# Kernel optimization log

Hardware: AMD Instinct MI355X
Metric: run time of the kernel (lower is better)

## Reference

```python
import jax, jax.numpy as jnp
import numpy as np

ALPHA = 0.25
GAMMA = 2.0
VAR = jnp.array([0.1, 0.1, 0.2, 0.2, 0.1, 0.1, 0.2, 0.2], dtype=jnp.float32)


def calc_iou(a, b):
    # a: [A,4] anchors, b: [M,4] gt boxes -> IoU [A,M]
    area = (b[:, 2] - b[:, 0]) * (b[:, 3] - b[:, 1])
    iw = jnp.maximum(jnp.minimum(a[:, 2:3], b[:, 2]) - jnp.maximum(a[:, 0:1], b[:, 0]), 0.0)
    ih = jnp.maximum(jnp.minimum(a[:, 3:4], b[:, 3]) - jnp.maximum(a[:, 1:2], b[:, 1]), 0.0)
    ua = jnp.maximum(((a[:, 2] - a[:, 0]) * (a[:, 3] - a[:, 1]))[:, None] + area - iw * ih, 1e-8)
    return iw * ih / ua


def _per_sample(cls_p, reg, anchor, ann1, ann2):
    A = anchor.shape[0]
    M = ann1.shape[0]
    C = cls_p.shape[1]
    clsp = jnp.clip(cls_p, 1e-4, 1.0 - 1e-4)
    iou = calc_iou(anchor, ann1[:, :4])               # [A,M]
    bto = jnp.max(iou, axis=1)                        # best_truth_overlap [A]
    bti = jnp.argmax(iou, axis=1)                     # best_truth_idx [A]
    bpi = jnp.argmax(iou, axis=0)                     # best_prior_idx [M]
    bto = bto.at[bpi].set(2.0)
    owner = jnp.full((A,), -1, jnp.int32).at[bpi].max(jnp.arange(M, dtype=jnp.int32))
    bti = jnp.where(owner >= 0, owner, bti.astype(jnp.int32))
    pos = bto >= 0.5
    neg = bto < 0.4
    assigned = ann1[bti]                              # [A,6]
    labels = assigned[:, 4].astype(jnp.int32)
    onehot = jax.nn.one_hot(labels, C, dtype=clsp.dtype)
    targets = jnp.where(neg[:, None], 0.0, -1.0)
    targets = jnp.where(pos[:, None], onehot, targets)
    af = jnp.where(targets == 1.0, ALPHA, 1.0 - ALPHA)
    fw = af * jnp.where(targets == 1.0, 1.0 - clsp, clsp) ** GAMMA
    bce = -(targets * jnp.log(clsp) + (1.0 - targets) * jnp.log(1.0 - clsp))
    cls_loss = jnp.where(targets != -1.0, fw * bce, 0.0)
    npos = jnp.sum(pos).astype(clsp.dtype)
    cls_out = cls_loss.sum() / jnp.maximum(npos, 1.0)

    aw = anchor[:, 2] - anchor[:, 0]
    ah = anchor[:, 3] - anchor[:, 1]
    acx = anchor[:, 0] + 0.5 * aw
    acy = anchor[:, 1] + 0.5 * ah
    # track-id first-match between frames (replaces nested python loops)
    match = assigned[:, 5][:, None] == ann2[:, 5][None, :]   # [A,M2]
    has = jnp.any(match, axis=1)
    first = jnp.argmax(match, axis=1)
    ann_next = jnp.where(has[:, None], ann2[first], 0.0)     # [A,6]
    gw0 = assigned[:, 2] - assigned[:, 0]
    gh0 = assigned[:, 3] - assigned[:, 1]
    gcx = assigned[:, 0] + 0.5 * gw0
    gcy = assigned[:, 1] + 0.5 * gh0
    gw = jnp.maximum(gw0, 1.0)
    gh = jnp.maximum(gh0, 1.0)
    nw0 = ann_next[:, 2] - ann_next[:, 0]
    nh0 = ann_next[:, 3] - ann_next[:, 1]
    ncx = ann_next[:, 0] + 0.5 * nw0
    ncy = ann_next[:, 1] + 0.5 * nh0
    nw = jnp.maximum(nw0, 1.0)
    nh = jnp.maximum(nh0, 1.0)
    t = jnp.stack([
        (gcx - acx) / aw, (gcy - acy) / ah, jnp.log(gw / aw), jnp.log(gh / ah),
        (ncx - acx) / aw, (ncy - acy) / ah, jnp.log(nw / aw), jnp.log(nh / ah)
    ], axis=1) / VAR                                          # [A,8]
    reg_mask = jnp.concatenate([
        jnp.ones((A, 4), clsp.dtype),
        jnp.broadcast_to(has[:, None], (A, 4)).astype(clsp.dtype)
    ], axis=1)
    diff = jnp.abs(t - reg) * reg_mask
    hub = jnp.where(diff <= 1.0 / 9.0, 0.5 * 9.0 * diff ** 2, diff - 0.5 / 9.0)
    reg_out = jnp.sum(hub * pos[:, None].astype(clsp.dtype)) / jnp.maximum(npos * 8.0, 1.0)
    return cls_out, reg_out


def reference(classifications, regressions, anchors, annotations1, annotations2):
    cl, rl = jax.vmap(_per_sample, in_axes=(0, 0, None, 0, 0))(
        classifications, regressions, anchors[0], annotations1, annotations2)
    return jnp.mean(cl, keepdims=True), jnp.mean(rl, keepdims=True)


def setup_inputs() -> dict:
    key = jax.random.key(0)
    ks = jax.random.split(key, 10)
    B, A, C, M = 8, 100000, 80, 32
    IMG = 512.0

    def rand_boxes(k, prefix):
        k1, k2 = jax.random.split(k)
        ctr = jax.random.uniform(k1, prefix + (2,), jnp.float32, 0.0, IMG)
        wh = jax.random.uniform(k2, prefix + (2,), jnp.float32, 16.0, 128.0)
        return jnp.concatenate([ctr - 0.5 * wh, ctr + 0.5 * wh], axis=-1)

    anchors = rand_boxes(ks[0], (1, A))
    classifications = jax.random.uniform(ks[1], (B, A, C), jnp.float32)
    regressions = jax.random.normal(ks[2], (B, A, 8), jnp.float32) * 0.1

    def make_ann(kb, ki):
        boxes = rand_boxes(kb, (B, M))
        lbl = jax.random.randint(ki, (B, M, 1), 0, C).astype(jnp.float32)
        tid = jax.random.randint(jax.random.fold_in(ki, 1), (B, M, 1), 0, 40).astype(jnp.float32)
        return jnp.concatenate([boxes, lbl, tid], axis=-1)

    annotations1 = make_ann(ks[3], ks[4])
    annotations2 = make_ann(ks[5], ks[6])
    return {"classifications": classifications, "regressions": regressions,
            "anchors": anchors, "annotations1": annotations1, "annotations2": annotations2}
```

## Files before the change

kernel.cpp:

```cpp
#include <hip/hip_runtime.h>

typedef unsigned long long ull;

#define MMAX 128

__global__ void k_init(ull* __restrict__ bpi, int* __restrict__ npos,
                       float* __restrict__ cls_sum, float* __restrict__ reg_sum,
                       int BM, int B) {
    int i = blockIdx.x * blockDim.x + threadIdx.x;
    if (i < BM) bpi[i] = 0ull;
    if (i < B) { npos[i] = 0; cls_sum[i] = 0.f; reg_sum[i] = 0.f; }
}

__global__ void k_iou(const float* __restrict__ anchors, const float* __restrict__ ann1,
                      float* __restrict__ bto, int* __restrict__ bti, ull* __restrict__ bpi,
                      int A, int M) {
    __shared__ float s_box[MMAX][4];
    __shared__ float s_area[MMAX];
    __shared__ ull s_part[4][MMAX];
    const int b = blockIdx.y;
    const int tid = threadIdx.x;
    for (int i = tid; i < M; i += blockDim.x) {
        const float* g = ann1 + ((size_t)b * M + i) * 6;
        float x1 = g[0], y1 = g[1], x2 = g[2], y2 = g[3];
        s_box[i][0] = x1; s_box[i][1] = y1; s_box[i][2] = x2; s_box[i][3] = y2;
        s_area[i] = (x2 - x1) * (y2 - y1);
    }
    __syncthreads();

    const int base = blockIdx.x * (blockDim.x * 4);
    float ax1[4], ay1[4], ax2[4], ay2[4], aar[4];
    int aidx[4]; bool val[4];
#pragma unroll
    for (int u = 0; u < 4; ++u) {
        int a = base + u * blockDim.x + tid;
        aidx[u] = a; val[u] = (a < A);
        float4 av = make_float4(0.f, 0.f, 0.f, 0.f);
        if (val[u]) av = ((const float4*)anchors)[a];
        ax1[u] = av.x; ay1[u] = av.y; ax2[u] = av.z; ay2[u] = av.w;
        aar[u] = (av.z - av.x) * (av.w - av.y);
    }
    float best[4] = {-1.f, -1.f, -1.f, -1.f};
    int bestj[4] = {0, 0, 0, 0};
    const int lane = tid & 63, wid = tid >> 6;

    for (int j = 0; j < M; ++j) {
        float bx1 = s_box[j][0], by1 = s_box[j][1], bx2 = s_box[j][2], by2 = s_box[j][3];
        float bar = s_area[j];
        ull key = 0ull;
#pragma unroll
        for (int u = 0; u < 4; ++u) {
            float iw = fmaxf(fminf(ax2[u], bx2) - fmaxf(ax1[u], bx1), 0.f);
            float ih = fmaxf(fminf(ay2[u], by2) - fmaxf(ay1[u], by1), 0.f);
            float inter = iw * ih;
            float ua = fmaxf(aar[u] + bar - inter, 1e-8f);
            float iou = inter / ua;
            if (val[u]) {
                if (iou > best[u]) { best[u] = iou; bestj[u] = j; }
                ull k2 = (((ull)__float_as_uint(iou)) << 32) | (ull)(0xFFFFFFFFu - (unsigned)aidx[u]);
                if (k2 > key) key = k2;
            }
        }
#pragma unroll
        for (int off = 32; off > 0; off >>= 1) {
            ull o = __shfl_down(key, off);
            if (o > key) key = o;
        }
        if (lane == 0) s_part[wid][j] = key;
    }
#pragma unroll
    for (int u = 0; u < 4; ++u) {
        if (val[u]) {
            bto[(size_t)b * A + aidx[u]] = best[u];
            bti[(size_t)b * A + aidx[u]] = bestj[u];
        }
    }
    __syncthreads();
    for (int j = tid; j < M; j += blockDim.x) {
        ull key = s_part[0][j];
        if (s_part[1][j] > key) key = s_part[1][j];
        if (s_part[2][j] > key) key = s_part[2][j];
        if (s_part[3][j] > key) key = s_part[3][j];
        atomicMax(&bpi[(size_t)b * M + j], key);
    }
}

__global__ void k_force(const ull* __restrict__ bpi, float* __restrict__ bto,
                        int* __restrict__ bti, int A, int M, int B) {
    int b = blockIdx.x * blockDim.x + threadIdx.x;
    if (b >= B) return;
    for (int j = 0; j < M; ++j) {
        ull key = bpi[(size_t)b * M + j];
        unsigned a = 0xFFFFFFFFu - (unsigned)(key & 0xFFFFFFFFull);
        bto[(size_t)b * A + a] = 2.0f;
        bti[(size_t)b * A + a] = j;
    }
}

template <int C4C>
__global__ void k_cls(const float* __restrict__ cls, const float* __restrict__ ann1,
                      const float* __restrict__ bto, const int* __restrict__ bti,
                      float* __restrict__ cls_sum, int A, int c4_rt, int M) {
    const int c4 = (C4C > 0) ? C4C : c4_rt;
    const int b = blockIdx.y;
    const int N4 = A * c4;
    const float4* cb = (const float4*)(cls + (size_t)b * A * (c4 * 4));
    const float* btob = bto + (size_t)b * A;
    const int* btib = bti + (size_t)b * A;
    const float* ann1b = ann1 + (size_t)b * M * 6;
    float lsum = 0.f;
    const int stride = gridDim.x * blockDim.x;
    for (int i = blockIdx.x * blockDim.x + threadIdx.x; i < N4; i += stride) {
        int a = i / c4;
        int c0 = (i - a * c4) * 4;
        float v = btob[a];
        bool pos = (v >= 0.5f), neg = (v < 0.4f);
        if (pos || neg) {
            float4 x = cb[i];
            int label = -1;
            if (pos) label = (int)ann1b[btib[a] * 6 + 4];
            float xs[4] = {x.x, x.y, x.z, x.w};
#pragma unroll
            for (int k = 0; k < 4; ++k) {
                float p = fminf(fmaxf(xs[k], 1e-4f), 1.0f - 1e-4f);
                if (pos && (c0 + k) == label) {
                    float q = 1.f - p;
                    lsum += 0.25f * q * q * (-__logf(p));
                } else {
                    lsum += 0.75f * p * p * (-__logf(1.f - p));
                }
            }
        }
    }
#pragma unroll
    for (int off = 32; off > 0; off >>= 1) lsum += __shfl_down(lsum, off);
    __shared__ float s_red[4];
    if ((threadIdx.x & 63) == 0) s_red[threadIdx.x >> 6] = lsum;
    __syncthreads();
    if (threadIdx.x == 0)
        atomicAdd(&cls_sum[b], s_red[0] + s_red[1] + s_red[2] + s_red[3]);
}

__global__ void k_reg(const float* __restrict__ anchors, const float* __restrict__ ann1,
                      const float* __restrict__ ann2, const float* __restrict__ regs,
                      const float* __restrict__ bto, const int* __restrict__ bti,
                      float* __restrict__ reg_sum, int* __restrict__ npos,
                      int A, int M, int M2) {
    __shared__ float s_a1[MMAX * 6];
    __shared__ float s_a2[MMAX * 6];
    const int b = blockIdx.y;
    const int tid = threadIdx.x;
    for (int i = tid; i < M * 6; i += blockDim.x) s_a1[i] = ann1[(size_t)b * M * 6 + i];
    for (int i = tid; i < M2 * 6; i += blockDim.x) s_a2[i] = ann2[(size_t)b * M2 * 6 + i];
    __syncthreads();

    const int a = blockIdx.x * blockDim.x + tid;
    float sum = 0.f;
    int cnt = 0;
    if (a < A) {
        float v = bto[(size_t)b * A + a];
        if (v >= 0.5f) {
            cnt = 1;
            const int ji = bti[(size_t)b * A + a];
            const float* as = &s_a1[ji * 6];
            float4 av = ((const float4*)anchors)[a];
            float aw = av.z - av.x, ah = av.w - av.y;
            float acx = av.x + 0.5f * aw, acy = av.y + 0.5f * ah;
            float gw0 = as[2] - as[0], gh0 = as[3] - as[1];
            float gcx = as[0] + 0.5f * gw0, gcy = as[1] + 0.5f * gh0;
            float gw = fmaxf(gw0, 1.f), gh = fmaxf(gh0, 1.f);
            float t[8];
            t[0] = ((gcx - acx) / aw) / 0.1f;
            t[1] = ((gcy - acy) / ah) / 0.1f;
            t[2] = __logf(gw / aw) / 0.2f;
            t[3] = __logf(gh / ah) / 0.2f;
            int nterm = 4;
            float tid5 = as[5];
            int first = -1;
            for (int j2 = 0; j2 < M2; ++j2) {
                if (s_a2[j2 * 6 + 5] == tid5) { first = j2; break; }
            }
            if (first >= 0) {
                const float* ns = &s_a2[first * 6];
                float nw0 = ns[2] - ns[0], nh0 = ns[3] - ns[1];
                float ncx = ns[0] + 0.5f * nw0, ncy = ns[1] + 0.5f * nh0;
                float nw = fmaxf(nw0, 1.f), nh = fmaxf(nh0, 1.f);
                t[4] = ((ncx - acx) / aw) / 0.1f;
                t[5] = ((ncy - acy) / ah) / 0.1f;
                t[6] = __logf(nw / aw) / 0.2f;
                t[7] = __logf(nh / ah) / 0.2f;
                nterm = 8;
            }
            const float* rg = regs + ((size_t)b * A + a) * 8;
            for (int k = 0; k < nterm; ++k) {
                float d = fabsf(t[k] - rg[k]);
                sum += (d <= (1.0f / 9.0f)) ? (4.5f * d * d) : (d - (0.5f / 9.0f));
            }
        }
    }
#pragma unroll
    for (int off = 32; off > 0; off >>= 1) {
        sum += __shfl_down(sum, off);
        cnt += __shfl_down(cnt, off);
    }
    __shared__ float s_rs[4];
    __shared__ int s_rc[4];
    if ((tid & 63) == 0) { s_rs[tid >> 6] = sum; s_rc[tid >> 6] = cnt; }
    __syncthreads();
    if (tid == 0) {
        atomicAdd(&reg_sum[b], s_rs[0] + s_rs[1] + s_rs[2] + s_rs[3]);
        atomicAdd(&npos[b], s_rc[0] + s_rc[1] + s_rc[2] + s_rc[3]);
    }
}

__global__ void k_final(const float* __restrict__ cls_sum, const float* __restrict__ reg_sum,
                        const int* __restrict__ npos, float* __restrict__ out, int B) {
    if (blockIdx.x == 0 && threadIdx.x == 0) {
        float c = 0.f, r = 0.f;
        for (int b = 0; b < B; ++b) {
            float np_ = (float)npos[b];
            c += cls_sum[b] / fmaxf(np_, 1.f);
            r += reg_sum[b] / fmaxf(np_ * 8.f, 1.f);
        }
        out[0] = c / (float)B;
        out[1] = r / (float)B;
    }
}

extern "C" void kernel_launch(void* const* d_in, const int* in_sizes, int n_in,
                              void* d_out, int out_size, void* d_ws, size_t ws_size,
                              hipStream_t stream) {
    const float* cls = (const float*)d_in[0];
    const float* regs = (const float*)d_in[1];
    const float* anchors = (const float*)d_in[2];
    const float* ann1 = (const float*)d_in[3];
    const float* ann2 = (const float*)d_in[4];
    float* out = (float*)d_out;

    const int A = in_sizes[2] / 4;
    const int B = in_sizes[1] / (A * 8);
    const int C = in_sizes[0] / (B * A);
    const int M = in_sizes[3] / (B * 6);
    const int M2 = in_sizes[4] / (B * 6);

    char* ws = (char*)d_ws;
    size_t off = 0;
    ull* bpi = (ull*)(ws + off);      off += (size_t)B * M * sizeof(ull);   off = (off + 255) & ~(size_t)255;
    int* npos = (int*)(ws + off);     off += (size_t)B * sizeof(int);       off = (off + 255) & ~(size_t)255;
    float* cls_sum = (float*)(ws + off); off += (size_t)B * sizeof(float);  off = (off + 255) & ~(size_t)255;
    float* reg_sum = (float*)(ws + off); off += (size_t)B * sizeof(float);  off = (off + 255) & ~(size_t)255;
    float* bto = (float*)(ws + off);  off += (size_t)B * A * sizeof(float); off = (off + 255) & ~(size_t)255;
    int* bti = (int*)(ws + off);      off += (size_t)B * A * sizeof(int);

    int initN = (B * M > B) ? B * M : B;
    k_init<<<dim3((initN + 255) / 256), dim3(256), 0, stream>>>(bpi, npos, cls_sum, reg_sum, B * M, B);

    dim3 g1((A + 1023) / 1024, B);
    k_iou<<<g1, dim3(256), 0, stream>>>(anchors, ann1, bto, bti, bpi, A, M);

    k_force<<<dim3(1), dim3(64), 0, stream>>>(bpi, bto, bti, A, M, B);

    dim3 g3(512, B);
    if (C % 4 == 0 && C / 4 == 20)
        k_cls<20><<<g3, dim3(256), 0, stream>>>(cls, ann1, bto, bti, cls_sum, A, C / 4, M);
    else
        k_cls<0><<<g3, dim3(256), 0, stream>>>(cls, ann1, bto, bti, cls_sum, A, C / 4, M);

    dim3 g4((A + 255) / 256, B);
    k_reg<<<g4, dim3(256), 0, stream>>>(anchors, ann1, ann2, regs, bto, bti, reg_sum, npos, A, M, M2);

    k_final<<<1, 1, 0, stream>>>(cls_sum, reg_sum, npos, out, B);
}
```

Baseline: 473.8 us.

## Fuse cls and reg loss kernels, replace atomics with per-block partials

Regression loss is folded into the classification kernel: the thread that handles the first class chunk of a positive anchor also computes that anchor's smooth-L1 terms. The separate init, force, reg and final kernels go away. Best-prior keys are written as per-block partials and reduced in a new assign kernel, which also computes npos from per-block positive counts plus a correction for forced anchors. Final normalisation is done with atomics straight into the output. The aim is fewer launches and one less pass over bto/bti, at the cost of MMAX dropping to 64 and some divergence in the fused loop.

```diff
diff --git a/kernel.cpp b/kernel.cpp
--- a/kernel.cpp
+++ b/kernel.cpp
@@ -2,23 +2,18 @@
 
 typedef unsigned long long ull;
 
-#define MMAX 128
-
-__global__ void k_init(ull* __restrict__ bpi, int* __restrict__ npos,
-                       float* __restrict__ cls_sum, float* __restrict__ reg_sum,
-                       int BM, int B) {
-    int i = blockIdx.x * blockDim.x + threadIdx.x;
-    if (i < BM) bpi[i] = 0ull;
-    if (i < B) { npos[i] = 0; cls_sum[i] = 0.f; reg_sum[i] = 0.f; }
-}
+#define MMAX 64
 
 __global__ void k_iou(const float* __restrict__ anchors, const float* __restrict__ ann1,
-                      float* __restrict__ bto, int* __restrict__ bti, ull* __restrict__ bpi,
-                      int A, int M) {
+                      float* __restrict__ bto, int* __restrict__ bti,
+                      ull* __restrict__ part_key, int* __restrict__ part_cnt,
+                      int A, int M, int NBLK) {
     __shared__ float s_box[MMAX][4];
     __shared__ float s_area[MMAX];
     __shared__ ull s_part[4][MMAX];
+    __shared__ int s_cnt[4];
     const int b = blockIdx.y;
+    const int blk = blockIdx.x;
     const int tid = threadIdx.x;
     for (int i = tid; i < M; i += blockDim.x) {
         const float* g = ann1 + ((size_t)b * M + i) * 6;
@@ -28,7 +23,7 @@
     }
     __syncthreads();
 
-    const int base = blockIdx.x * (blockDim.x * 4);
+    const int base = blk * (blockDim.x * 4);
     float ax1[4], ay1[4], ax2[4], ay2[4], aar[4];
     int aidx[4]; bool val[4];
 #pragma unroll
@@ -68,57 +63,97 @@
         }
         if (lane == 0) s_part[wid][j] = key;
     }
+    int cnt = 0;
 #pragma unroll
     for (int u = 0; u < 4; ++u) {
         if (val[u]) {
             bto[(size_t)b * A + aidx[u]] = best[u];
             bti[(size_t)b * A + aidx[u]] = bestj[u];
-        }
-    }
-    __syncthreads();
-    for (int j = tid; j < M; j += blockDim.x) {
-        ull key = s_part[0][j];
-        if (s_part[1][j] > key) key = s_part[1][j];
-        if (s_part[2][j] > key) key = s_part[2][j];
-        if (s_part[3][j] > key) key = s_part[3][j];
-        atomicMax(&bpi[(size_t)b * M + j], key);
-    }
-}
-
-__global__ void k_force(const ull* __restrict__ bpi, float* __restrict__ bto,
-                        int* __restrict__ bti, int A, int M, int B) {
-    int b = blockIdx.x * blockDim.x + threadIdx.x;
-    if (b >= B) return;
-    for (int j = 0; j < M; ++j) {
-        ull key = bpi[(size_t)b * M + j];
-        unsigned a = 0xFFFFFFFFu - (unsigned)(key & 0xFFFFFFFFull);
-        bto[(size_t)b * A + a] = 2.0f;
-        bti[(size_t)b * A + a] = j;
-    }
+            if (best[u] >= 0.5f) ++cnt;
+        }
+    }
+#pragma unroll
+    for (int off = 32; off > 0; off >>= 1) cnt += __shfl_down(cnt, off);
+    if (lane == 0) s_cnt[wid] = cnt;
+    __syncthreads();
+    if (tid < M) {
+        ull key = s_part[0][tid];
+        if (s_part[1][tid] > key) key = s_part[1][tid];
+        if (s_part[2][tid] > key) key = s_part[2][tid];
+        if (s_part[3][tid] > key) key = s_part[3][tid];
+        part_key[((size_t)b * NBLK + blk) * M + tid] = key;
+    }
+    if (tid == 0) part_cnt[b * NBLK + blk] = s_cnt[0] + s_cnt[1] + s_cnt[2] + s_cnt[3];
+}
+
+__global__ void k_assign(const ull* __restrict__ part_key, const int* __restrict__ part_cnt,
+                         float* __restrict__ bto, int* __restrict__ bti,
+                         int* __restrict__ npos, float* __restrict__ out,
+                         int A, int M, int NBLK) {
+    const int b = blockIdx.x;
+    const int tid = threadIdx.x;
+    __shared__ int s_a[MMAX];
+    if (tid < M) {
+        ull key = 0ull;
+        for (int k = 0; k < NBLK; ++k) {
+            ull v = part_key[((size_t)b * NBLK + k) * M + tid];
+            if (v > key) key = v;
+        }
+        s_a[tid] = (int)(0xFFFFFFFFu - (unsigned)(key & 0xFFFFFFFFull));
+    }
+    __syncthreads();
+    int corr = 0;
+    if (tid < M) {
+        int a = s_a[tid];
+        bool owner = true;
+        for (int j2 = tid + 1; j2 < M; ++j2)
+            if (s_a[j2] == a) owner = false;
+        if (owner) {
+            float pre = bto[(size_t)b * A + a];
+            bto[(size_t)b * A + a] = 2.0f;
+            bti[(size_t)b * A + a] = tid;
+            if (pre < 0.5f) corr = 1;
+        }
+    }
+    int cnt = corr;
+    for (int k = tid; k < NBLK; k += 64) cnt += part_cnt[b * NBLK + k];
+#pragma unroll
+    for (int off = 32; off > 0; off >>= 1) cnt += __shfl_down(cnt, off);
+    if (tid == 0) npos[b] = cnt;
+    if (b == 0 && tid == 0) { out[0] = 0.f; out[1] = 0.f; }
 }
 
 template <int C4C>
-__global__ void k_cls(const float* __restrict__ cls, const float* __restrict__ ann1,
-                      const float* __restrict__ bto, const int* __restrict__ bti,
-                      float* __restrict__ cls_sum, int A, int c4_rt, int M) {
+__global__ __launch_bounds__(256, 4)
+void k_main(const float* __restrict__ cls, const float* __restrict__ regs,
+            const float* __restrict__ anchors,
+            const float* __restrict__ ann1, const float* __restrict__ ann2,
+            const float* __restrict__ bto, const int* __restrict__ bti,
+            const int* __restrict__ npos, float* __restrict__ out,
+            int A, int c4_rt, int M, int M2, float invB) {
     const int c4 = (C4C > 0) ? C4C : c4_rt;
     const int b = blockIdx.y;
+    const int tid = threadIdx.x;
+    __shared__ float s_a1[MMAX * 6];
+    __shared__ float s_a2[MMAX * 6];
+    for (int i = tid; i < M * 6; i += blockDim.x) s_a1[i] = ann1[(size_t)b * M * 6 + i];
+    for (int i = tid; i < M2 * 6; i += blockDim.x) s_a2[i] = ann2[(size_t)b * M2 * 6 + i];
+    __syncthreads();
+
     const int N4 = A * c4;
     const float4* cb = (const float4*)(cls + (size_t)b * A * (c4 * 4));
     const float* btob = bto + (size_t)b * A;
     const int* btib = bti + (size_t)b * A;
-    const float* ann1b = ann1 + (size_t)b * M * 6;
-    float lsum = 0.f;
+    float lsum = 0.f, rsum = 0.f;
     const int stride = gridDim.x * blockDim.x;
-    for (int i = blockIdx.x * blockDim.x + threadIdx.x; i < N4; i += stride) {
+    for (int i = blockIdx.x * blockDim.x + tid; i < N4; i += stride) {
         int a = i / c4;
         int c0 = (i - a * c4) * 4;
         float v = btob[a];
         bool pos = (v >= 0.5f), neg = (v < 0.4f);
         if (pos || neg) {
             float4 x = cb[i];
-            int label = -1;
-            if (pos) label = (int)ann1b[btib[a] * 6 + 4];
+            int label = pos ? (int)s_a1[btib[a] * 6 + 4] : -1;
             float xs[4] = {x.x, x.y, x.z, x.w};
 #pragma unroll
             for (int k = 0; k < 4; ++k) {
@@ -131,37 +166,8 @@
                 }
             }
         }
-    }
-#pragma unroll
-    for (int off = 32; off > 0; off >>= 1) lsum += __shfl_down(lsum, off);
-    __shared__ float s_red[4];
-    if ((threadIdx.x & 63) == 0) s_red[threadIdx.x >> 6] = lsum;
-    __syncthreads();
-    if (threadIdx.x == 0)
-        atomicAdd(&cls_sum[b], s_red[0] + s_red[1] + s_red[2] + s_red[3]);
-}
-
-__global__ void k_reg(const float* __restrict__ anchors, const float* __restrict__ ann1,
-                      const float* __restrict__ ann2, const float* __restrict__ regs,
-                      const float* __restrict__ bto, const int* __restrict__ bti,
-                      float* __restrict__ reg_sum, int* __restrict__ npos,
-                      int A, int M, int M2) {
-    __shared__ float s_a1[MMAX * 6];
-    __shared__ float s_a2[MMAX * 6];
-    const int b = blockIdx.y;
-    const int tid = threadIdx.x;
-    for (int i = tid; i < M * 6; i += blockDim.x) s_a1[i] = ann1[(size_t)b * M * 6 + i];
-    for (int i = tid; i < M2 * 6; i += blockDim.x) s_a2[i] = ann2[(size_t)b * M2 * 6 + i];
-    __syncthreads();
-
-    const int a = blockIdx.x * blockDim.x + tid;
-    float sum = 0.f;
-    int cnt = 0;
-    if (a < A) {
-        float v = bto[(size_t)b * A + a];
-        if (v >= 0.5f) {
-            cnt = 1;
-            const int ji = bti[(size_t)b * A + a];
+        if (pos && c0 == 0) {
+            const int ji = btib[a];
             const float* as = &s_a1[ji * 6];
             float4 av = ((const float4*)anchors)[a];
             float aw = av.z - av.x, ah = av.w - av.y;
@@ -194,36 +200,24 @@
             const float* rg = regs + ((size_t)b * A + a) * 8;
             for (int k = 0; k < nterm; ++k) {
                 float d = fabsf(t[k] - rg[k]);
-                sum += (d <= (1.0f / 9.0f)) ? (4.5f * d * d) : (d - (0.5f / 9.0f));
+                rsum += (d <= (1.0f / 9.0f)) ? (4.5f * d * d) : (d - (0.5f / 9.0f));
             }
         }
     }
 #pragma unroll
     for (int off = 32; off > 0; off >>= 1) {
-        sum += __shfl_down(sum, off);
-        cnt += __shfl_down(cnt, off);
-    }
-    __shared__ float s_rs[4];
-    __shared__ int s_rc[4];
-    if ((tid & 63) == 0) { s_rs[tid >> 6] = sum; s_rc[tid >> 6] = cnt; }
+        lsum += __shfl_down(lsum, off);
+        rsum += __shfl_down(rsum, off);
+    }
+    __shared__ float s_l[4], s_r[4];
+    if ((tid & 63) == 0) { s_l[tid >> 6] = lsum; s_r[tid >> 6] = rsum; }
     __syncthreads();
     if (tid == 0) {
-        atomicAdd(&reg_sum[b], s_rs[0] + s_rs[1] + s_rs[2] + s_rs[3]);
-        atomicAdd(&npos[b], s_rc[0] + s_rc[1] + s_rc[2] + s_rc[3]);
-    }
-}
-
-__global__ void k_final(const float* __restrict__ cls_sum, const float* __restrict__ reg_sum,
-                        const int* __restrict__ npos, float* __restrict__ out, int B) {
-    if (blockIdx.x == 0 && threadIdx.x == 0) {
-        float c = 0.f, r = 0.f;
-        for (int b = 0; b < B; ++b) {
-            float np_ = (float)npos[b];
-            c += cls_sum[b] / fmaxf(np_, 1.f);
-            r += reg_sum[b] / fmaxf(np_ * 8.f, 1.f);
-        }
-        out[0] = c / (float)B;
-        out[1] = r / (float)B;
+        float np_ = (float)npos[b];
+        float l = (s_l[0] + s_l[1] + s_l[2] + s_l[3]) / fmaxf(np_, 1.f) * invB;
+        float r = (s_r[0] + s_r[1] + s_r[2] + s_r[3]) / fmaxf(np_ * 8.f, 1.f) * invB;
+        atomicAdd(&out[0], l);
+        atomicAdd(&out[1], r);
     }
 }
 
@@ -242,32 +236,27 @@
     const int C = in_sizes[0] / (B * A);
     const int M = in_sizes[3] / (B * 6);
     const int M2 = in_sizes[4] / (B * 6);
+    const int NBLK = (A + 1023) / 1024;
 
     char* ws = (char*)d_ws;
     size_t off = 0;
-    ull* bpi = (ull*)(ws + off);      off += (size_t)B * M * sizeof(ull);   off = (off + 255) & ~(size_t)255;
-    int* npos = (int*)(ws + off);     off += (size_t)B * sizeof(int);       off = (off + 255) & ~(size_t)255;
-    float* cls_sum = (float*)(ws + off); off += (size_t)B * sizeof(float);  off = (off + 255) & ~(size_t)255;
-    float* reg_sum = (float*)(ws + off); off += (size_t)B * sizeof(float);  off = (off + 255) & ~(size_t)255;
-    float* bto = (float*)(ws + off);  off += (size_t)B * A * sizeof(float); off = (off + 255) & ~(size_t)255;
-    int* bti = (int*)(ws + off);      off += (size_t)B * A * sizeof(int);
-
-    int initN = (B * M > B) ? B * M : B;
-    k_init<<<dim3((initN + 255) / 256), dim3(256), 0, stream>>>(bpi, npos, cls_sum, reg_sum, B * M, B);
-
-    dim3 g1((A + 1023) / 1024, B);
-    k_iou<<<g1, dim3(256), 0, stream>>>(anchors, ann1, bto, bti, bpi, A, M);
-
-    k_force<<<dim3(1), dim3(64), 0, stream>>>(bpi, bto, bti, A, M, B);
+    float* bto = (float*)(ws + off);     off += (size_t)B * A * sizeof(float);        off = (off + 255) & ~(size_t)255;
+    int* bti = (int*)(ws + off);         off += (size_t)B * A * sizeof(int);          off = (off + 255) & ~(size_t)255;
+    ull* part_key = (ull*)(ws + off);    off += (size_t)B * NBLK * M * sizeof(ull);   off = (off + 255) & ~(size_t)255;
+    int* part_cnt = (int*)(ws + off);    off += (size_t)B * NBLK * sizeof(int);       off = (off + 255) & ~(size_t)255;
+    int* npos = (int*)(ws + off);        off += (size_t)B * sizeof(int);
+
+    dim3 g1(NBLK, B);
+    k_iou<<<g1, dim3(256), 0, stream>>>(anchors, ann1, bto, bti, part_key, part_cnt, A, M, NBLK);
+
+    k_assign<<<dim3(B), dim3(64), 0, stream>>>(part_key, part_cnt, bto, bti, npos, out, A, M, NBLK);
 
     dim3 g3(512, B);
-    if (C % 4 == 0 && C / 4 == 20)
-        k_cls<20><<<g3, dim3(256), 0, stream>>>(cls, ann1, bto, bti, cls_sum, A, C / 4, M);
+    const float invB = 1.0f / (float)B;
+    if (C == 80)
+        k_main<20><<<g3, dim3(256), 0, stream>>>(cls, regs, anchors, ann1, ann2, bto, bti,
+                                                 npos, out, A, C / 4, M, M2, invB);
     else
-        k_cls<0><<<g3, dim3(256), 0, stream>>>(cls, ann1, bto, bti, cls_sum, A, C / 4, M);
-
-    dim3 g4((A + 255) / 256, B);
-    k_reg<<<g4, dim3(256), 0, stream>>>(anchors, ann1, ann2, regs, bto, bti, reg_sum, npos, A, M, M2);
-
-    k_final<<<1, 1, 0, stream>>>(cls_sum, reg_sum, npos, out, B);
-}
+        k_main<0><<<g3, dim3(256), 0, stream>>>(cls, regs, anchors, ann1, ann2, bto, bti,
+                                                npos, out, A, C / 4, M, M2, invB);
+}
```

New measurement: 504.9 us. +6.6%, slower.
